# Kernel tuning notes

Measured on AMD Instinct MI355X. Metric: run time of the kernel, lower is better.

The kernel has to match this reference:

```python
import jax, jax.numpy as jnp
import numpy as np

N, E, F_IN, HID, HEADS, G = 50000, 800000, 128, 128, 4, 512
NEG_SLOPE = 0.2


def setup_inputs() -> dict:
    key = jax.random.key(0)
    ks = jax.random.split(key, 16)
    x = jax.random.normal(ks[0], (N, F_IN), dtype=jnp.float32)
    edge_index = jax.random.randint(ks[1], (2, E), 0, N, dtype=jnp.int32)
    batch = jnp.sort(jax.random.randint(ks[2], (N,), 0, G, dtype=jnp.int32))
    s1 = 1.0 / np.sqrt(F_IN)
    s2 = 1.0 / np.sqrt(HEADS * HID)
    params = {
        "W1": jax.random.uniform(ks[3], (F_IN, HEADS * HID), jnp.float32, -s1, s1),
        "a_src1": jax.random.normal(ks[4], (HEADS, HID), jnp.float32) * s1,
        "a_dst1": jax.random.normal(ks[5], (HEADS, HID), jnp.float32) * s1,
        "b1": jnp.zeros((HEADS * HID,), jnp.float32),
        "W2": jax.random.uniform(ks[6], (HEADS * HID, HID), jnp.float32, -s2, s2),
        "a_src2": jax.random.normal(ks[7], (1, HID), jnp.float32) * s2,
        "a_dst2": jax.random.normal(ks[8], (1, HID), jnp.float32) * s2,
        "b2": jnp.zeros((HID,), jnp.float32),
        "Wl": jax.random.normal(ks[9], (HID, 1), jnp.float32) / np.sqrt(HID),
        "bl": jnp.zeros((1,), jnp.float32),
    }
    return dict(x=x, edge_index=edge_index, batch=batch, **params)


def _gat_conv(x, W, a_src, a_dst, b, src, dst, heads, out_ch):
    n = x.shape[0]
    h = (x @ W).reshape(n, heads, out_ch)                      # [N,H,C]
    asrc = jnp.sum(h * a_src, axis=-1)                          # [N,H]
    adst = jnp.sum(h * a_dst, axis=-1)                          # [N,H]
    logits = jax.nn.leaky_relu(asrc[src] + adst[dst], NEG_SLOPE)  # [E,H]
    m = jax.ops.segment_max(logits, dst, num_segments=n)        # stable softmax per dst
    e = jnp.exp(logits - m[dst])
    denom = jax.ops.segment_sum(e, dst, num_segments=n)
    alpha = e / denom[dst]                                      # [E,H]
    out = jax.ops.segment_sum(alpha[:, :, None] * h[src], dst, num_segments=n)
    return out.reshape(n, heads * out_ch) + b


def reference(x, edge_index, batch, W1, a_src1, a_dst1, b1, W2, a_src2, a_dst2, b2, Wl, bl):
    n = x.shape[0]
    loop = jnp.arange(n, dtype=edge_index.dtype)
    src = jnp.concatenate([edge_index[0], loop])  # add_self_loops=True (PyG default)
    dst = jnp.concatenate([edge_index[1], loop])
    h = _gat_conv(x, W1, a_src1, a_dst1, b1, src, dst, HEADS, HID)
    h = jax.nn.elu(h)
    h = _gat_conv(h, W2, a_src2, a_dst2, b2, src, dst, 1, HID)
    h = jax.nn.elu(h)
    # global_mean_pool
    sums = jax.ops.segment_sum(h, batch, num_segments=G)
    cnts = jax.ops.segment_sum(jnp.ones((n,), h.dtype), batch, num_segments=G)
    pooled = sums / jnp.maximum(cnts, 1.0)[:, None]
    return (pooled @ Wl + bl).squeeze()
```

## Files before the change

### kernel.cpp

```cpp
#include <hip/hip_runtime.h>
#include <math.h>

#define NEG_SLOPE 0.2f

typedef float f4 __attribute__((ext_vector_type(4)));
typedef __attribute__((ext_vector_type(8))) short short8;
typedef __attribute__((ext_vector_type(4))) float f32x4;
typedef unsigned short ushort_t;
typedef unsigned char uchar_t;

__device__ __forceinline__ float bf2f(unsigned short s) {
    unsigned u = ((unsigned)s) << 16;
    float f; __builtin_memcpy(&f, &u, 4); return f;
}
__device__ __forceinline__ unsigned short f2bf(float f) {
    unsigned u; __builtin_memcpy(&u, &f, 4);
    u = (u + 0x7FFFu + ((u >> 16) & 1u)) >> 16;
    return (unsigned short)u;
}
__device__ __forceinline__ void gload16(const void* g, void* l) {
    __builtin_amdgcn_global_load_lds((const __attribute__((address_space(1))) void*)g,
                                     (__attribute__((address_space(3))) void*)l, 16, 0, 0);
}
__device__ __forceinline__ void cvt4(unsigned u, float& a, float& b, float& c, float& d) {
    asm("v_cvt_f32_ubyte0 %0, %1" : "=v"(a) : "v"(u));
    asm("v_cvt_f32_ubyte1 %0, %1" : "=v"(b) : "v"(u));
    asm("v_cvt_f32_ubyte2 %0, %1" : "=v"(c) : "v"(u));
    asm("v_cvt_f32_ubyte3 %0, %1" : "=v"(d) : "v"(u));
}

__global__ void hist_kernel(const int* __restrict__ ei, int E, int Et, int* __restrict__ deg) {
    int e = blockIdx.x * blockDim.x + threadIdx.x;
    if (e >= Et) return;
    int d = (e < E) ? ei[E + e] : (e - E);
    atomicAdd(&deg[d], 1);
}

__global__ __launch_bounds__(1024) void scan_local(const int* __restrict__ deg,
                                                   int* __restrict__ off,
                                                   int* __restrict__ btot, int n) {
    __shared__ int s_w[16];
    int tid = threadIdx.x, lane = tid & 63, wv = tid >> 6;
    int i = blockIdx.x * 1024 + tid;
    int v = (i < n) ? deg[i] : 0;
    int x = v;
    #pragma unroll
    for (int d = 1; d < 64; d <<= 1) {
        int y = __shfl_up(x, d);
        if (lane >= d) x += y;
    }
    if (lane == 63) s_w[wv] = x;
    __syncthreads();
    if (tid < 16) {
        int y = s_w[tid];
        int z = y;
        #pragma unroll
        for (int d = 1; d < 16; d <<= 1) {
            int t2 = __shfl_up(z, d);
            if (tid >= d) z += t2;
        }
        if (tid == 15) btot[blockIdx.x] = z;
        s_w[tid] = z - y;
    }
    __syncthreads();
    if (i < n) off[i] = s_w[wv] + (x - v);
}

__global__ void scan_base(int* __restrict__ btot, int nb) {
    int lane = threadIdx.x;
    int v = (lane < nb) ? btot[lane] : 0;
    int x = v;
    #pragma unroll
    for (int d = 1; d < 64; d <<= 1) {
        int y = __shfl_up(x, d);
        if (lane >= d) x += y;
    }
    int total = __shfl(x, nb - 1);
    if (lane < nb) btot[lane] = x - v;
    if (lane == 0) btot[nb] = total;
}

__global__ void scan_add(const int* __restrict__ btot, int* __restrict__ off,
                         int* __restrict__ cur, const int* __restrict__ batch,
                         int* __restrict__ gcnt, int n, int nb) {
    int i = blockIdx.x * blockDim.x + threadIdx.x;
    if (i < n) {
        int o = off[i] + btot[i >> 10];
        off[i] = o;
        cur[i] = o;
        atomicAdd(&gcnt[batch[i]], 1);
    } else if (i == n) {
        off[n] = btot[nb];
    }
}

__global__ void scatter_kernel(const int* __restrict__ ei, int E, int Et,
                               int* __restrict__ cur, int* __restrict__ csr) {
    int e = blockIdx.x * blockDim.x + threadIdx.x;
    if (e >= Et) return;
    int s, d;
    if (e < E) { s = ei[e]; d = ei[E + e]; }
    else       { s = d = e - E; }
    int p = atomicAdd(&cur[d], 1);
    csr[p] = s;
}

__global__ void cast_all(const float* __restrict__ x, const float* __restrict__ W1,
                         const float* __restrict__ W2, ushort_t* __restrict__ xb,
                         ushort_t* __restrict__ W1t, ushort_t* __restrict__ W2t,
                         int n_x, int pad_x) {
    int i = blockIdx.x * blockDim.x + threadIdx.x;
    if (i < pad_x) {
        xb[i] = f2bf(i < n_x ? x[i] : 0.f);
        return;
    }
    int k = i - pad_x;
    if (k < 128 * 512) {
        int r = k >> 9, c = k & 511;
        W1t[(size_t)c * 128 + r] = f2bf(W1[k]);
        return;
    }
    k -= 128 * 512;
    if (k < 512 * 128) {
        int r = k >> 7, c = k & 127;
        W2t[(size_t)c * 512 + r] = f2bf(W2[k]);
    }
}

template<int H>
__global__ __launch_bounds__(256) void gemm_q128(const ushort_t* __restrict__ A,
                                                 const ushort_t* __restrict__ Bt,
                                                 uchar_t* __restrict__ Cq,
                                                 const float* __restrict__ aw_src,
                                                 const float* __restrict__ aw_dst,
                                                 float* __restrict__ side,
                                                 float* __restrict__ avd,
                                                 int K) {
    const int Nc = H * 128;
    __shared__ __align__(16) ushort_t As[128 * 32];
    __shared__ __align__(16) ushort_t Bs[128 * 32];
    __shared__ float s_red[3][2][128];
    __shared__ float s_rs[128];
    __shared__ __align__(16) uchar_t s_q[128 * 144];
    const int t = threadIdx.x, w = t >> 6, lane = t & 63;
    const int r0 = blockIdx.x * 128, hb = blockIdx.y, c0 = hb * 128;
    const int wr = w & 1, wc = w >> 1;

    const ushort_t* Ag = A + (size_t)(r0 + w * 32 + (lane >> 2)) * K + (lane & 3) * 8;
    const ushort_t* Bg = Bt + (size_t)(c0 + w * 32 + (lane >> 2)) * K + (lane & 3) * 8;
    ushort_t* Al = As + w * 1024;
    ushort_t* Bl = Bs + w * 1024;

    f32x4 acc[4][4] = {};
    for (int k0 = 0; k0 < K; k0 += 32) {
        __syncthreads();
        gload16(Ag + k0, Al);
        gload16(Ag + k0 + (size_t)16 * K, Al + 512);
        gload16(Bg + k0, Bl);
        gload16(Bg + k0 + (size_t)16 * K, Bl + 512);
        __syncthreads();
        short8 af[4], bf[4];
        #pragma unroll
        for (int i = 0; i < 4; i++) {
            af[i] = *(const short8*)(As + (wr * 64 + i * 16 + (lane & 15)) * 32 + (lane >> 4) * 8);
            bf[i] = *(const short8*)(Bs + (wc * 64 + i * 16 + (lane & 15)) * 32 + (lane >> 4) * 8);
        }
        #pragma unroll
        for (int i = 0; i < 4; i++)
            #pragma unroll
            for (int jj = 0; jj < 4; jj++)
                acc[i][jj] = __builtin_amdgcn_mfma_f32_16x16x32_bf16(af[i], bf[jj], acc[i][jj], 0, 0, 0);
    }

    float asc[4], adc[4];
    #pragma unroll
    for (int jj = 0; jj < 4; jj++) {
        int c = c0 + wc * 64 + jj * 16 + (lane & 15);
        asc[jj] = aw_src[c];
        adc[jj] = aw_dst[c];
    }
    #pragma unroll
    for (int i = 0; i < 4; i++) {
        #pragma unroll
        for (int r = 0; r < 4; r++) {
            float m = 0.f, ps = 0.f, pd = 0.f;
            #pragma unroll
            for (int jj = 0; jj < 4; jj++) {
                float v = acc[i][jj][r];
                m = fmaxf(m, fabsf(v));
                ps = fmaf(v, asc[jj], ps);
                pd = fmaf(v, adc[jj], pd);
            }
            #pragma unroll
            for (int d = 1; d < 16; d <<= 1) {
                m = fmaxf(m, __shfl_xor(m, d));
                ps += __shfl_xor(ps, d);
                pd += __shfl_xor(pd, d);
            }
            if ((lane & 15) == 0) {
                int row = wr * 64 + i * 16 + (lane >> 4) * 4 + r;
                s_red[0][wc][row] = m;
                s_red[1][wc][row] = ps;
                s_red[2][wc][row] = pd;
            }
        }
    }
    __syncthreads();
    if (t < 128) {
        float rm = fmaxf(fmaxf(s_red[0][0][t], s_red[0][1][t]), 1e-30f);
        s_rs[t] = 127.f / rm;
        int node = r0 + t;
        side[(size_t)node * (2 * H) + hb]     = s_red[1][0][t] + s_red[1][1][t];
        side[(size_t)node * (2 * H) + H + hb] = rm * (1.f / 127.f);
        avd[(size_t)node * H + hb]            = s_red[2][0][t] + s_red[2][1][t];
    }
    __syncthreads();
    #pragma unroll
    for (int i = 0; i < 4; i++)
        #pragma unroll
        for (int jj = 0; jj < 4; jj++)
            #pragma unroll
            for (int r = 0; r < 4; r++) {
                int row = wr * 64 + i * 16 + (lane >> 4) * 4 + r;
                int col = wc * 64 + jj * 16 + (lane & 15);
                int qi = (int)rintf(acc[i][jj][r] * s_rs[row]) + 128;
                qi = min(255, max(0, qi));
                s_q[row * 144 + col] = (uchar_t)qi;
            }
    __syncthreads();
    #pragma unroll
    for (int p2 = 0; p2 < 4; p2++) {
        int idx = p2 * 256 + t;
        int row = idx >> 3, ch = idx & 7;
        *(uint4*)(Cq + (size_t)(r0 + row) * Nc + c0 + ch * 16) =
            *(const uint4*)(s_q + row * 144 + ch * 16);
    }
}

template<int H, int TOT, bool OUT_BF16>
__global__ __launch_bounds__(256) void agg_q(const int* __restrict__ off,
                                             const int* __restrict__ csr,
                                             const uchar_t* __restrict__ fq,
                                             const float* __restrict__ side,
                                             const float* __restrict__ avd,
                                             const float* __restrict__ bias,
                                             void* __restrict__ outv, int n) {
    constexpr int J = TOT / 64;
    __shared__ float s_e[4][64 * H];
    __shared__ float s_es[4][64 * H];
    int w = threadIdx.x >> 6, lane = threadIdx.x & 63;
    int dst = blockIdx.x * 4 + w;
    if (dst >= n) return;
    const int h_own = (H == 1) ? 0 : (lane >> 4);
    float adv[H];
    if constexpr (H == 4) {
        f4 t4 = *(const f4*)&avd[(size_t)dst * 4];
        #pragma unroll
        for (int h = 0; h < 4; h++) adv[h] = t4[h];
    } else {
        adv[0] = avd[dst];
    }
    int beg = off[dst], end = off[dst + 1];
    float den = 0.f, Ssum = 0.f;
    float acc[J] = {};
    float* ew  = s_e[w];
    float* esw = s_es[w];

    for (int b = beg; b < end; b += 64) {
        int idx = b + lane;
        bool val = idx < end;
        int sv = val ? csr[idx] : 0;
        unsigned myoff = (unsigned)sv * TOT;
        if constexpr (H == 4) {
            const f4* sp = (const f4*)(side + (size_t)sv * 8);
            f4 av = sp[0], sc = sp[1];
            f4 ev, esv;
            #pragma unroll
            for (int h = 0; h < 4; h++) {
                float l = av[h] + adv[h];
                l = fmaxf(l, l * NEG_SLOPE);
                float e = val ? __expf(l) : 0.f;
                ev[h] = e;
                esv[h] = e * sc[h];
            }
            *(f4*)&ew[lane * 4]  = ev;
            *(f4*)&esw[lane * 4] = esv;
        } else {
            float2 sp = *(const float2*)(side + (size_t)sv * 2);
            float l = sp.x + adv[0];
            l = fmaxf(l, l * NEG_SLOPE);
            float e = val ? __expf(l) : 0.f;
            ew[lane]  = e;
            esw[lane] = e * sp.y;
        }
        asm volatile("s_waitcnt lgkmcnt(0)" ::: "memory");
        int cnt = min(64, end - b);
        for (int jb = 0; jb < cnt; jb += 8) {
            uint2 u8v[8];
            unsigned us16[8];
            #pragma unroll
            for (int q = 0; q < 8; q++) {
                unsigned o = (unsigned)__builtin_amdgcn_readlane((int)myoff, jb + q);
                if constexpr (J == 8) {
                    u8v[q] = *(const uint2*)(fq + o + lane * 8);
                } else {
                    us16[q] = *(const ushort_t*)(fq + o + lane * 2);
                }
            }
            #pragma unroll
            for (int q = 0; q < 8; q++) {
                int j = jb + q;
                float e  = ew[j * H + h_own];
                float es = esw[j * H + h_own];
                den += e;
                Ssum += es;
                if constexpr (J == 8) {
                    float b0, b1, b2, b3;
                    cvt4(u8v[q].x, b0, b1, b2, b3);
                    acc[0] = fmaf(es, b0, acc[0]);
                    acc[1] = fmaf(es, b1, acc[1]);
                    acc[2] = fmaf(es, b2, acc[2]);
                    acc[3] = fmaf(es, b3, acc[3]);
                    cvt4(u8v[q].y, b0, b1, b2, b3);
                    acc[4] = fmaf(es, b0, acc[4]);
                    acc[5] = fmaf(es, b1, acc[5]);
                    acc[6] = fmaf(es, b2, acc[6]);
                    acc[7] = fmaf(es, b3, acc[7]);
                } else {
                    float b0, b1;
                    asm("v_cvt_f32_ubyte0 %0, %1" : "=v"(b0) : "v"(us16[q]));
                    asm("v_cvt_f32_ubyte1 %0, %1" : "=v"(b1) : "v"(us16[q]));
                    acc[0] = fmaf(es, b0, acc[0]);
                    acc[1] = fmaf(es, b1, acc[1]);
                }
            }
        }
    }
    float rden = 1.f / den;
    if constexpr (OUT_BF16) {
        unsigned short ov[J];
        #pragma unroll
        for (int u = 0; u < J; u++) {
            float v = (acc[u] - 128.f * Ssum) * rden + bias[lane * J + u];
            v = v > 0.f ? v : expm1f(v);
            ov[u] = f2bf(v);
        }
        *(short8*)((ushort_t*)outv + (size_t)dst * TOT + lane * J) = *(short8*)ov;
    } else {
        float v0 = (acc[0] - 128.f * Ssum) * rden + bias[lane * 2];
        float v1 = (acc[1] - 128.f * Ssum) * rden + bias[lane * 2 + 1];
        v0 = v0 > 0.f ? v0 : expm1f(v0);
        v1 = v1 > 0.f ? v1 : expm1f(v1);
        float2 vv = make_float2(v0, v1);
        *(float2*)((float*)outv + (size_t)dst * TOT + lane * 2) = vv;
    }
}

__global__ __launch_bounds__(256) void pool_kernel(const float* __restrict__ feat,
                                                   const int* __restrict__ batch,
                                                   float* __restrict__ gsum, int n) {
    int t = threadIdx.x;
    int ch = t & 127, half = t >> 7;
    int base = blockIdx.x * 64;
    float acc = 0.f;
    int curg = -1;
    for (int k = half; k < 64; k += 2) {
        int node = base + k;
        if (node >= n) break;
        int g = batch[node];
        if (g != curg) {
            if (curg >= 0) atomicAdd(&gsum[(size_t)curg * 128 + ch], acc);
            acc = 0.f;
            curg = g;
        }
        acc += feat[(size_t)node * 128 + ch];
    }
    if (curg >= 0) atomicAdd(&gsum[(size_t)curg * 128 + ch], acc);
}

__global__ __launch_bounds__(256) void final_kernel(const float* __restrict__ gsum,
                                                    const int* __restrict__ gcnt,
                                                    const float* __restrict__ Wl,
                                                    const float* __restrict__ bl,
                                                    float* __restrict__ out, int g_total) {
    int w = threadIdx.x >> 6, lane = threadIdx.x & 63;
    int g = blockIdx.x * 4 + w;
    if (g >= g_total) return;
    float inv = 1.f / fmaxf((float)gcnt[g], 1.f);
    float p = 0.f;
    #pragma unroll
    for (int j = 0; j < 2; j++) {
        int ch = lane + 64 * j;
        p += gsum[(size_t)g * 128 + ch] * Wl[ch];
    }
    #pragma unroll
    for (int d = 32; d; d >>= 1) p += __shfl_xor(p, d);
    if (lane == 0) out[g] = p * inv + bl[0];
}

extern "C" void kernel_launch(void* const* d_in, const int* in_sizes, int n_in,
                              void* d_out, int out_size, void* d_ws, size_t ws_size,
                              hipStream_t stream) {
    const float* x   = (const float*)d_in[0];
    const int*   ei  = (const int*)d_in[1];
    const int*   bat = (const int*)d_in[2];
    const float* W1  = (const float*)d_in[3];
    const float* as1 = (const float*)d_in[4];
    const float* ad1 = (const float*)d_in[5];
    const float* b1  = (const float*)d_in[6];
    const float* W2  = (const float*)d_in[7];
    const float* as2 = (const float*)d_in[8];
    const float* ad2 = (const float*)d_in[9];
    const float* b2  = (const float*)d_in[10];
    const float* Wl  = (const float*)d_in[11];
    const float* bl  = (const float*)d_in[12];
    float* out = (float*)d_out;

    const int N    = in_sizes[0] / 128;
    const int E    = in_sizes[1] / 2;
    const int Et   = E + N;
    const int G    = 512;
    const int Mpad = (N + 127) & ~127;
    const int nb   = (N + 1023) >> 10;

    char* p = (char*)d_ws;
    auto alloc = [&](size_t bytes) { char* r = p; p += (bytes + 255) & ~(size_t)255; return r; };
    ushort_t* xb    = (ushort_t*)alloc((size_t)Mpad * 128 * 2);
    ushort_t* W1t   = (ushort_t*)alloc((size_t)512 * 128 * 2);
    ushort_t* W2t   = (ushort_t*)alloc((size_t)128 * 512 * 2);
    uchar_t*  h1q   = (uchar_t*)alloc((size_t)Mpad * 512);
    ushort_t* hb    = (ushort_t*)alloc((size_t)Mpad * 512 * 2);
    uchar_t*  h2q   = (uchar_t*)alloc((size_t)Mpad * 128);
    float*    feat2 = (float*)alloc((size_t)N * 128 * 4);
    float*    side1 = (float*)alloc((size_t)Mpad * 8 * 4);
    float*    avd1  = (float*)alloc((size_t)Mpad * 4 * 4);
    float*    side2 = (float*)alloc((size_t)Mpad * 2 * 4);
    float*    avd2  = (float*)alloc((size_t)Mpad * 4);
    float*    gsum  = (float*)alloc((size_t)G * 128 * 4);
    int*      gcnt  = (int*)alloc((size_t)G * 4);
    int*      deg   = (int*)alloc((size_t)N * 4);
    int*      off   = (int*)alloc((size_t)(N + 1) * 4);
    int*      cur   = (int*)alloc((size_t)N * 4);
    int*      btot  = (int*)alloc((size_t)128 * 4);
    int*      csr   = (int*)alloc((size_t)Et * 4);

    hipMemsetAsync(gsum, 0, (size_t)((char*)off - (char*)gsum), stream);
    hipMemsetAsync(hb + (size_t)N * 512, 0, (size_t)(Mpad - N) * 512 * 2, stream);

    hist_kernel<<<(Et + 255) / 256, 256, 0, stream>>>(ei, E, Et, deg);
    scan_local<<<nb, 1024, 0, stream>>>(deg, off, btot, N);
    scan_base<<<1, 64, 0, stream>>>(btot, nb);
    scan_add<<<(N + 256) / 256, 256, 0, stream>>>(btot, off, cur, bat, gcnt, N, nb);
    cast_all<<<((Mpad * 128 + 2 * 65536) + 255) / 256, 256, 0, stream>>>(x, W1, W2, xb, W1t, W2t,
                                                                         N * 128, Mpad * 128);
    scatter_kernel<<<(Et + 255) / 256, 256, 0, stream>>>(ei, E, Et, cur, csr);

    gemm_q128<4><<<dim3(Mpad / 128, 4), 256, 0, stream>>>(xb, W1t, h1q, as1, ad1, side1, avd1, 128);
    agg_q<4, 512, true><<<(N + 3) / 4, 256, 0, stream>>>(off, csr, h1q, side1, avd1, b1, hb, N);

    gemm_q128<1><<<dim3(Mpad / 128, 1), 256, 0, stream>>>(hb, W2t, h2q, as2, ad2, side2, avd2, 512);
    agg_q<1, 128, false><<<(N + 3) / 4, 256, 0, stream>>>(off, csr, h2q, side2, avd2, b2, feat2, N);

    pool_kernel<<<(N + 63) / 64, 256, 0, stream>>>(feat2, bat, gsum, N);
    final_kernel<<<(G + 3) / 4, 256, 0, stream>>>(gsum, gcnt, Wl, bl, out, G);
}
```

Before: 435.8 us.

## Merge preprocessing kernels and shrink layer-2 GEMM tile for more blocks

The degree histogram is folded into the cast kernel and the single-wave block-base scan is folded into scan_add, which removes two kernel launches and their serialization gaps. The GEMM is templated on the row-tile size so that the layer-2 projection (one 128-column block) uses 64-row tiles, doubling the grid to fill more CUs. The trade-offs are lower per-block data reuse in layer 2, every scan_add block redundantly rescanning btot, and the histogram atomics now sharing threads with the cast work.

```diff
diff --git a/kernel.cpp b/kernel.cpp
--- a/kernel.cpp
+++ b/kernel.cpp
@@ -9,10 +9,6 @@
 typedef unsigned short ushort_t;
 typedef unsigned char uchar_t;
 
-__device__ __forceinline__ float bf2f(unsigned short s) {
-    unsigned u = ((unsigned)s) << 16;
-    float f; __builtin_memcpy(&f, &u, 4); return f;
-}
 __device__ __forceinline__ unsigned short f2bf(float f) {
     unsigned u; __builtin_memcpy(&u, &f, 4);
     u = (u + 0x7FFFu + ((u >> 16) & 1u)) >> 16;
@@ -29,11 +25,31 @@
     asm("v_cvt_f32_ubyte3 %0, %1" : "=v"(d) : "v"(u));
 }
 
-__global__ void hist_kernel(const int* __restrict__ ei, int E, int Et, int* __restrict__ deg) {
-    int e = blockIdx.x * blockDim.x + threadIdx.x;
-    if (e >= Et) return;
-    int d = (e < E) ? ei[E + e] : (e - E);
-    atomicAdd(&deg[d], 1);
+__global__ void prep_kernel(const float* __restrict__ x, const float* __restrict__ W1,
+                            const float* __restrict__ W2, ushort_t* __restrict__ xb,
+                            ushort_t* __restrict__ W1t, ushort_t* __restrict__ W2t,
+                            const int* __restrict__ ei, int* __restrict__ deg,
+                            int n_x, int pad_x, int E, int Et) {
+    int i = blockIdx.x * blockDim.x + threadIdx.x;
+    if (i < Et) {
+        int d = (i < E) ? ei[E + i] : (i - E);
+        atomicAdd(&deg[d], 1);
+    }
+    if (i < pad_x) {
+        xb[i] = f2bf(i < n_x ? x[i] : 0.f);
+        return;
+    }
+    int k = i - pad_x;
+    if (k < 128 * 512) {
+        int r = k >> 9, c = k & 511;
+        W1t[(size_t)c * 128 + r] = f2bf(W1[k]);
+        return;
+    }
+    k -= 128 * 512;
+    if (k < 512 * 128) {
+        int r = k >> 7, c = k & 127;
+        W2t[(size_t)c * 512 + r] = f2bf(W2[k]);
+    }
 }
 
 __global__ __launch_bounds__(1024) void scan_local(const int* __restrict__ deg,
@@ -66,31 +82,35 @@
     if (i < n) off[i] = s_w[wv] + (x - v);
 }
 
-__global__ void scan_base(int* __restrict__ btot, int nb) {
-    int lane = threadIdx.x;
-    int v = (lane < nb) ? btot[lane] : 0;
-    int x = v;
-    #pragma unroll
-    for (int d = 1; d < 64; d <<= 1) {
-        int y = __shfl_up(x, d);
-        if (lane >= d) x += y;
-    }
-    int total = __shfl(x, nb - 1);
-    if (lane < nb) btot[lane] = x - v;
-    if (lane == 0) btot[nb] = total;
-}
-
-__global__ void scan_add(const int* __restrict__ btot, int* __restrict__ off,
-                         int* __restrict__ cur, const int* __restrict__ batch,
-                         int* __restrict__ gcnt, int n, int nb) {
-    int i = blockIdx.x * blockDim.x + threadIdx.x;
+__global__ __launch_bounds__(256) void scan_add(const int* __restrict__ btot,
+                                                int* __restrict__ off,
+                                                int* __restrict__ cur,
+                                                const int* __restrict__ batch,
+                                                int* __restrict__ gcnt, int n, int nb) {
+    __shared__ int s_b[2];
+    int i = blockIdx.x * 256 + threadIdx.x;
+    if (threadIdx.x < 64) {
+        int lane = threadIdx.x;
+        int v = (lane < nb) ? btot[lane] : 0;
+        int x = v;
+        #pragma unroll
+        for (int d = 1; d < 64; d <<= 1) {
+            int y = __shfl_up(x, d);
+            if (lane >= d) x += y;
+        }
+        int c = blockIdx.x >> 2;
+        int base = (c == 0) ? 0 : __shfl(x, c - 1);
+        int total = __shfl(x, nb - 1);
+        if (lane == 0) { s_b[0] = base; s_b[1] = total; }
+    }
+    __syncthreads();
     if (i < n) {
-        int o = off[i] + btot[i >> 10];
+        int o = off[i] + s_b[0];
         off[i] = o;
         cur[i] = o;
         atomicAdd(&gcnt[batch[i]], 1);
     } else if (i == n) {
-        off[n] = btot[nb];
+        off[n] = s_b[1];
     }
 }
 
@@ -105,68 +125,49 @@
     csr[p] = s;
 }
 
-__global__ void cast_all(const float* __restrict__ x, const float* __restrict__ W1,
-                         const float* __restrict__ W2, ushort_t* __restrict__ xb,
-                         ushort_t* __restrict__ W1t, ushort_t* __restrict__ W2t,
-                         int n_x, int pad_x) {
-    int i = blockIdx.x * blockDim.x + threadIdx.x;
-    if (i < pad_x) {
-        xb[i] = f2bf(i < n_x ? x[i] : 0.f);
-        return;
-    }
-    int k = i - pad_x;
-    if (k < 128 * 512) {
-        int r = k >> 9, c = k & 511;
-        W1t[(size_t)c * 128 + r] = f2bf(W1[k]);
-        return;
-    }
-    k -= 128 * 512;
-    if (k < 512 * 128) {
-        int r = k >> 7, c = k & 127;
-        W2t[(size_t)c * 512 + r] = f2bf(W2[k]);
-    }
-}
-
-template<int H>
-__global__ __launch_bounds__(256) void gemm_q128(const ushort_t* __restrict__ A,
-                                                 const ushort_t* __restrict__ Bt,
-                                                 uchar_t* __restrict__ Cq,
-                                                 const float* __restrict__ aw_src,
-                                                 const float* __restrict__ aw_dst,
-                                                 float* __restrict__ side,
-                                                 float* __restrict__ avd,
-                                                 int K) {
+template<int MI, int H>
+__global__ __launch_bounds__(256) void gemm_q(const ushort_t* __restrict__ A,
+                                              const ushort_t* __restrict__ Bt,
+                                              uchar_t* __restrict__ Cq,
+                                              const float* __restrict__ aw_src,
+                                              const float* __restrict__ aw_dst,
+                                              float* __restrict__ side,
+                                              float* __restrict__ avd,
+                                              int K) {
+    constexpr int BM = MI * 32;
+    constexpr int AI = MI / 2;
     const int Nc = H * 128;
-    __shared__ __align__(16) ushort_t As[128 * 32];
+    __shared__ __align__(16) ushort_t As[BM * 32];
     __shared__ __align__(16) ushort_t Bs[128 * 32];
-    __shared__ float s_red[3][2][128];
-    __shared__ float s_rs[128];
-    __shared__ __align__(16) uchar_t s_q[128 * 144];
+    __shared__ float s_red[3][2][BM];
+    __shared__ float s_rs[BM];
+    __shared__ __align__(16) uchar_t s_q[BM * 144];
     const int t = threadIdx.x, w = t >> 6, lane = t & 63;
-    const int r0 = blockIdx.x * 128, hb = blockIdx.y, c0 = hb * 128;
+    const int r0 = blockIdx.x * BM, hb = blockIdx.y, c0 = hb * 128;
     const int wr = w & 1, wc = w >> 1;
 
-    const ushort_t* Ag = A + (size_t)(r0 + w * 32 + (lane >> 2)) * K + (lane & 3) * 8;
+    const ushort_t* Ag = A + (size_t)(r0 + w * (BM / 4) + (lane >> 2)) * K + (lane & 3) * 8;
     const ushort_t* Bg = Bt + (size_t)(c0 + w * 32 + (lane >> 2)) * K + (lane & 3) * 8;
-    ushort_t* Al = As + w * 1024;
+    ushort_t* Al = As + w * (BM / 4) * 32;
     ushort_t* Bl = Bs + w * 1024;
 
-    f32x4 acc[4][4] = {};
+    f32x4 acc[MI][4] = {};
     for (int k0 = 0; k0 < K; k0 += 32) {
         __syncthreads();
-        gload16(Ag + k0, Al);
-        gload16(Ag + k0 + (size_t)16 * K, Al + 512);
+        #pragma unroll
+        for (int m = 0; m < AI; m++) gload16(Ag + k0 + (size_t)m * 16 * K, Al + m * 512);
         gload16(Bg + k0, Bl);
         gload16(Bg + k0 + (size_t)16 * K, Bl + 512);
         __syncthreads();
-        short8 af[4], bf[4];
-        #pragma unroll
-        for (int i = 0; i < 4; i++) {
-            af[i] = *(const short8*)(As + (wr * 64 + i * 16 + (lane & 15)) * 32 + (lane >> 4) * 8);
-            bf[i] = *(const short8*)(Bs + (wc * 64 + i * 16 + (lane & 15)) * 32 + (lane >> 4) * 8);
-        }
-        #pragma unroll
-        for (int i = 0; i < 4; i++)
+        short8 af[MI], bf[4];
+        #pragma unroll
+        for (int i = 0; i < MI; i++)
+            af[i] = *(const short8*)(As + (wr * MI * 16 + i * 16 + (lane & 15)) * 32 + (lane >> 4) * 8);
+        #pragma unroll
+        for (int jj = 0; jj < 4; jj++)
+            bf[jj] = *(const short8*)(Bs + (wc * 64 + jj * 16 + (lane & 15)) * 32 + (lane >> 4) * 8);
+        #pragma unroll
+        for (int i = 0; i < MI; i++)
             #pragma unroll
             for (int jj = 0; jj < 4; jj++)
                 acc[i][jj] = __builtin_amdgcn_mfma_f32_16x16x32_bf16(af[i], bf[jj], acc[i][jj], 0, 0, 0);
@@ -180,7 +181,7 @@
         adc[jj] = aw_dst[c];
     }
     #pragma unroll
-    for (int i = 0; i < 4; i++) {
+    for (int i = 0; i < MI; i++) {
         #pragma unroll
         for (int r = 0; r < 4; r++) {
             float m = 0.f, ps = 0.f, pd = 0.f;
@@ -198,7 +199,7 @@
                 pd += __shfl_xor(pd, d);
             }
             if ((lane & 15) == 0) {
-                int row = wr * 64 + i * 16 + (lane >> 4) * 4 + r;
+                int row = wr * MI * 16 + i * 16 + (lane >> 4) * 4 + r;
                 s_red[0][wc][row] = m;
                 s_red[1][wc][row] = ps;
                 s_red[2][wc][row] = pd;
@@ -206,7 +207,7 @@
         }
     }
     __syncthreads();
-    if (t < 128) {
+    if (t < BM) {
         float rm = fmaxf(fmaxf(s_red[0][0][t], s_red[0][1][t]), 1e-30f);
         s_rs[t] = 127.f / rm;
         int node = r0 + t;
@@ -216,12 +217,12 @@
     }
     __syncthreads();
     #pragma unroll
-    for (int i = 0; i < 4; i++)
+    for (int i = 0; i < MI; i++)
         #pragma unroll
         for (int jj = 0; jj < 4; jj++)
             #pragma unroll
             for (int r = 0; r < 4; r++) {
-                int row = wr * 64 + i * 16 + (lane >> 4) * 4 + r;
+                int row = wr * MI * 16 + i * 16 + (lane >> 4) * 4 + r;
                 int col = wc * 64 + jj * 16 + (lane & 15);
                 int qi = (int)rintf(acc[i][jj][r] * s_rs[row]) + 128;
                 qi = min(255, max(0, qi));
@@ -229,7 +230,7 @@
             }
     __syncthreads();
     #pragma unroll
-    for (int p2 = 0; p2 < 4; p2++) {
+    for (int p2 = 0; p2 < BM / 32; p2++) {
         int idx = p2 * 256 + t;
         int row = idx >> 3, ch = idx & 7;
         *(uint4*)(Cq + (size_t)(r0 + row) * Nc + c0 + ch * 16) =
@@ -447,18 +448,17 @@
     hipMemsetAsync(gsum, 0, (size_t)((char*)off - (char*)gsum), stream);
     hipMemsetAsync(hb + (size_t)N * 512, 0, (size_t)(Mpad - N) * 512 * 2, stream);
 
-    hist_kernel<<<(Et + 255) / 256, 256, 0, stream>>>(ei, E, Et, deg);
+    const int prep_n = Mpad * 128 + 2 * 65536;
+    prep_kernel<<<(prep_n + 255) / 256, 256, 0, stream>>>(x, W1, W2, xb, W1t, W2t,
+                                                          ei, deg, N * 128, Mpad * 128, E, Et);
     scan_local<<<nb, 1024, 0, stream>>>(deg, off, btot, N);
-    scan_base<<<1, 64, 0, stream>>>(btot, nb);
     scan_add<<<(N + 256) / 256, 256, 0, stream>>>(btot, off, cur, bat, gcnt, N, nb);
-    cast_all<<<((Mpad * 128 + 2 * 65536) + 255) / 256, 256, 0, stream>>>(x, W1, W2, xb, W1t, W2t,
-                                                                         N * 128, Mpad * 128);
     scatter_kernel<<<(Et + 255) / 256, 256, 0, stream>>>(ei, E, Et, cur, csr);
 
-    gemm_q128<4><<<dim3(Mpad / 128, 4), 256, 0, stream>>>(xb, W1t, h1q, as1, ad1, side1, avd1, 128);
+    gemm_q<4, 4><<<dim3(Mpad / 128, 4), 256, 0, stream>>>(xb, W1t, h1q, as1, ad1, side1, avd1, 128);
     agg_q<4, 512, true><<<(N + 3) / 4, 256, 0, stream>>>(off, csr, h1q, side1, avd1, b1, hb, N);
 
-    gemm_q128<1><<<dim3(Mpad / 128, 1), 256, 0, stream>>>(hb, W2t, h2q, as2, ad2, side2, avd2, 512);
+    gemm_q<2, 1><<<dim3(Mpad / 64, 1), 256, 0, stream>>>(hb, W2t, h2q, as2, ad2, side2, avd2, 512);
     agg_q<1, 128, false><<<(N + 3) / 4, 256, 0, stream>>>(off, csr, h2q, side2, avd2, b2, feat2, N);
 
     pool_kernel<<<(N + 63) / 64, 256, 0, stream>>>(feat2, bat, gsum, N);
```

Result: faster. 425.5 us (-2.4%).
